# Kernel tuning notes

Hardware: AMD Instinct MI355X
Metric: run time of the kernel (lower is better)

The kernel has to match this reference:

```python
import jax, jax.numpy as jnp
import numpy as np

EMBED = 1024  # embed_dim = hidden_dim = out_dim (n_head=1)
NQ, NK = 4096, 4096
NEG = 1e16


def setup_inputs() -> dict:
    key = jax.random.key(0)
    ks = jax.random.split(key, 10)
    stdv = 1.0 / np.sqrt(EMBED)
    lin = lambda kk: jax.random.uniform(kk, (EMBED, EMBED), jnp.float32, -stdv, stdv)
    vec = lambda kk: jax.random.uniform(kk, (EMBED,), jnp.float32, -stdv, stdv)
    return {
        "q": jax.random.normal(ks[0], (NQ, EMBED), jnp.float32),
        "k": jax.random.normal(ks[1], (NK, EMBED), jnp.float32),
        "mask": jax.random.randint(ks[2], (NQ, NK), 0, 2, jnp.int32),
        "wei": jax.random.uniform(ks[3], (NQ, NK), jnp.float32),
        "Wq": lin(ks[4]), "bq": vec(ks[5]),
        "Wk": lin(ks[6]), "bk": vec(ks[7]),
        "Wp": lin(ks[8]), "bp": vec(ks[9]),
    }


def reference(q, k, mask, wei, Wq, bq, Wk, bk, Wp, bp):
    # Linear projections (torch Linear: x @ W.T + b)
    kx = k @ Wk.T + bk                      # [NK, D]
    qx = q @ Wq.T + bq                      # [NQ, D]
    # dot_product score
    score = qx @ kx.T                       # [NQ, NK]
    bias = (mask.astype(jnp.int32) - 1).astype(score.dtype) * NEG
    score = jax.nn.softmax(score + bias, axis=-1)
    # second weighted+masked softmax pass
    score = jax.nn.softmax(score * wei + bias, axis=-1)
    out = (score @ kx) @ Wp.T + bp          # [NQ, D]
    return out, score
```

## Files before the change

### kernel.cpp

```cpp
#include <hip/hip_runtime.h>


typedef __bf16 bf16;
typedef __bf16 bf16x8 __attribute__((ext_vector_type(8)));
typedef __bf16 bf16x4 __attribute__((ext_vector_type(4)));
typedef float  f32x4  __attribute__((ext_vector_type(4)));
typedef float  f32x16 __attribute__((ext_vector_type(16)));
typedef int    i32x4  __attribute__((ext_vector_type(4)));

typedef __attribute__((address_space(1))) void as1_void;
typedef __attribute__((address_space(3))) void as3_void;

#define NQ  4096
#define NKK 4096
#define EMB 1024

#define BM 128
#define BN 128
#define BK 32

__device__ __forceinline__ void gld_lds16(const void* g, void* l) {
    __builtin_amdgcn_global_load_lds((as1_void*)g, (as3_void*)l, 16, 0, 0);
}

__global__ __launch_bounds__(256) void prep_all(
    const float* __restrict__ q, const float* __restrict__ k,
    const float* __restrict__ Wq, const float* __restrict__ Wk, const float* __restrict__ Wp,
    bf16* __restrict__ qh, bf16* __restrict__ ql,
    bf16* __restrict__ kh, bf16* __restrict__ kl,
    bf16* __restrict__ Wqh, bf16* __restrict__ Wql,
    bf16* __restrict__ Wkh, bf16* __restrict__ Wkl,
    bf16* __restrict__ Wph, bf16* __restrict__ Wpl,
    int nqk, int nw)
{
    const int z = blockIdx.y;
    const float* s; bf16* h; bf16* l; int n;
    switch (z) {
        case 0:  s = q;  h = qh;  l = ql;  n = nqk; break;
        case 1:  s = k;  h = kh;  l = kl;  n = nqk; break;
        case 2:  s = Wq; h = Wqh; l = Wql; n = nw;  break;
        case 3:  s = Wk; h = Wkh; l = Wkl; n = nw;  break;
        default: s = Wp; h = Wph; l = Wpl; n = nw;  break;
    }
    const int i = (blockIdx.x * 256 + threadIdx.x) * 4;
    if (i >= n) return;
    f32x4 v = *(const f32x4*)(s + i);
    bf16x4 hv, lv;
#pragma unroll
    for (int c = 0; c < 4; c++) {
        float x = v[c];
        bf16 hh = (bf16)x;
        hv[c] = hh;
        lv[c] = (bf16)(x - (float)hh);
    }
    *(bf16x4*)(h + i) = hv;
    *(bf16x4*)(l + i) = lv;
}

template<int NS, int MODE>
__global__ __launch_bounds__(256) void reduce_k(
    const float* __restrict__ P, const float* __restrict__ bias,
    float* __restrict__ of, bf16* __restrict__ oh, int n, int Nld)
{
    const int i = (blockIdx.x * 256 + threadIdx.x) * 4;
    if (i >= n) return;
    f32x4 v = *(const f32x4*)(P + i);
#pragma unroll
    for (int s = 1; s < NS; s++)
        v += *(const f32x4*)(P + (size_t)s * n + i);
    if (MODE == 1)
        v += *(const f32x4*)(bias + (i & (Nld - 1)));
    if (MODE == 0) {
        bf16x4 o;
#pragma unroll
        for (int c = 0; c < 4; c++) o[c] = (bf16)v[c];
        *(bf16x4*)(oh + i) = o;
    } else {
        *(f32x4*)(of + i) = v;
    }
}

template<int NSPLIT, int HAS_BIAS, int OUT_BF16>
__global__ __launch_bounds__(256) void gemm_bt(
    const bf16* __restrict__ A, const bf16* __restrict__ B,
    const float* __restrict__ bias,
    float* __restrict__ Cf, bf16* __restrict__ Cb,
    int M, int N, int Ksub, int lda, int ldb)
{
    __shared__ bf16 sA[BM * BK];
    __shared__ bf16 sB[BN * BK];
    const int t    = threadIdx.x;
    const int wave = t >> 6;
    const int lane = t & 63;
    const int l31  = lane & 31;
    const int lhi  = lane >> 5;
    const int wm   = wave >> 1;
    const int wn   = wave & 1;
    const int bm   = blockIdx.y * BM;
    const int bn   = blockIdx.x * BN;
    const int srow = t >> 2;
    const int gseg = (t & 3) ^ ((srow >> 1) & 3) ^ ((srow >> 3) & 3);
    const int rsw  = ((l31 >> 1) & 3) ^ ((l31 >> 3) & 3);
    const int kz   = (NSPLIT > 0) ? (int)blockIdx.z : 0;

    A += (size_t)kz * Ksub;
    B += (size_t)kz * Ksub;
    if (NSPLIT > 0) Cf += (size_t)kz * M * N;

    const bf16* ga = A + (size_t)(bm + srow) * lda + gseg * 8;
    const bf16* gb = B + (size_t)(bn + srow) * ldb + gseg * 8;
    char* lA = (char*)sA + wave * 1024;
    char* lB = (char*)sB + wave * 1024;

    f32x16 acc[2][2] = {};

    for (int k0 = 0; k0 < Ksub; k0 += BK) {
        __syncthreads();
        gld_lds16(ga + k0,                      lA);
        gld_lds16(ga + (size_t)64 * lda + k0,   lA + 4096);
        gld_lds16(gb + k0,                      lB);
        gld_lds16(gb + (size_t)64 * ldb + k0,   lB + 4096);
        __syncthreads();
        bf16x8 af[2][2], bfr[2][2];
#pragma unroll
        for (int mi = 0; mi < 2; mi++)
#pragma unroll
            for (int kh = 0; kh < 2; kh++)
                af[mi][kh] = *(const bf16x8*)
                    &sA[(wm * 64 + mi * 32 + l31) * BK + ((kh * 2 + lhi) ^ rsw) * 8];
#pragma unroll
        for (int nj = 0; nj < 2; nj++)
#pragma unroll
            for (int kh = 0; kh < 2; kh++)
                bfr[nj][kh] = *(const bf16x8*)
                    &sB[(wn * 64 + nj * 32 + l31) * BK + ((kh * 2 + lhi) ^ rsw) * 8];
#pragma unroll
        for (int kh = 0; kh < 2; kh++)
#pragma unroll
            for (int mi = 0; mi < 2; mi++)
#pragma unroll
                for (int nj = 0; nj < 2; nj++)
                    acc[mi][nj] = __builtin_amdgcn_mfma_f32_32x32x16_bf16(
                        af[mi][kh], bfr[nj][kh], acc[mi][nj], 0, 0, 0);
    }

#pragma unroll
    for (int mi = 0; mi < 2; mi++)
#pragma unroll
        for (int nj = 0; nj < 2; nj++) {
            const int cg = bn + wn * 64 + nj * 32 + l31;
            const float bv = HAS_BIAS ? bias[cg] : 0.0f;
#pragma unroll
            for (int r = 0; r < 16; r++) {
                const int rg = bm + wm * 64 + mi * 32 + (r & 3) + 8 * (r >> 2) + 4 * lhi;
                const float v = acc[mi][nj][r] + bv;
                const size_t idx = (size_t)rg * N + cg;
                if (NSPLIT > 0)    Cf[idx] = v;
                else if (OUT_BF16) Cb[idx] = (bf16)v;
                else               Cf[idx] = v;
            }
        }
}

template<int BATCH, int HAS_BIAS, int HILO>
__global__ __launch_bounds__(256) void gemm_bt_split(
    const bf16* __restrict__ Ah0, const bf16* __restrict__ Al0,
    const bf16* __restrict__ Bh0, const bf16* __restrict__ Bl0,
    const float* __restrict__ bias0, bf16* __restrict__ Ch0, bf16* __restrict__ Cl0,
    const bf16* __restrict__ Ah1, const bf16* __restrict__ Al1,
    const bf16* __restrict__ Bh1, const bf16* __restrict__ Bl1,
    const float* __restrict__ bias1, bf16* __restrict__ Ch1, bf16* __restrict__ Cl1,
    float* __restrict__ Cf,
    int M, int N, int K)
{
    __shared__ bf16 sAh[BM * BK], sAl[BM * BK], sBh[BN * BK], sBl[BN * BK];
    const int t    = threadIdx.x;
    const int wave = t >> 6;
    const int lane = t & 63;
    const int l31  = lane & 31;
    const int lhi  = lane >> 5;
    const int wm   = wave >> 1;
    const int wn   = wave & 1;
    const int bm   = blockIdx.y * BM;
    const int bn   = blockIdx.x * BN;
    const int srow = t >> 2;
    const int gseg = (t & 3) ^ ((srow >> 1) & 3) ^ ((srow >> 3) & 3);
    const int rsw  = ((l31 >> 1) & 3) ^ ((l31 >> 3) & 3);

    const int mt = BATCH ? (int)blockIdx.z : 0;

    const bf16* Ah = (BATCH && mt) ? Ah1 : Ah0;
    const bf16* Al = (BATCH && mt) ? Al1 : Al0;
    const bf16* Bh = (BATCH && mt) ? Bh1 : Bh0;
    const bf16* Bl = (BATCH && mt) ? Bl1 : Bl0;
    const float* bias = (BATCH && mt) ? bias1 : bias0;
    bf16* Ch = (BATCH && mt) ? Ch1 : Ch0;
    bf16* Cl = (BATCH && mt) ? Cl1 : Cl0;

    const size_t offA = (size_t)(bm + srow) * K + gseg * 8;
    const size_t offB = (size_t)(bn + srow) * K + gseg * 8;
    char* lAh = (char*)sAh + wave * 1024;
    char* lAl = (char*)sAl + wave * 1024;
    char* lBh = (char*)sBh + wave * 1024;
    char* lBl = (char*)sBl + wave * 1024;

    f32x16 acc[2][2] = {};

    for (int k0 = 0; k0 < K; k0 += BK) {
        __syncthreads();
        gld_lds16(Ah + offA + k0,                  lAh);
        gld_lds16(Ah + offA + (size_t)64 * K + k0, lAh + 4096);
        gld_lds16(Al + offA + k0,                  lAl);
        gld_lds16(Al + offA + (size_t)64 * K + k0, lAl + 4096);
        gld_lds16(Bh + offB + k0,                  lBh);
        gld_lds16(Bh + offB + (size_t)64 * K + k0, lBh + 4096);
        gld_lds16(Bl + offB + k0,                  lBl);
        gld_lds16(Bl + offB + (size_t)64 * K + k0, lBl + 4096);
        __syncthreads();
#pragma unroll
        for (int kh = 0; kh < 2; kh++) {
            const int ksw = ((kh * 2 + lhi) ^ rsw) * 8;
            bf16x8 ah[2], al[2], bh2[2], bl2[2];
#pragma unroll
            for (int mi = 0; mi < 2; mi++) {
                const int ro = (wm * 64 + mi * 32 + l31) * BK + ksw;
                ah[mi] = *(const bf16x8*)&sAh[ro];
                al[mi] = *(const bf16x8*)&sAl[ro];
            }
#pragma unroll
            for (int nj = 0; nj < 2; nj++) {
                const int ro = (wn * 64 + nj * 32 + l31) * BK + ksw;
                bh2[nj] = *(const bf16x8*)&sBh[ro];
                bl2[nj] = *(const bf16x8*)&sBl[ro];
            }
#pragma unroll
            for (int mi = 0; mi < 2; mi++)
#pragma unroll
                for (int nj = 0; nj < 2; nj++) {
                    acc[mi][nj] = __builtin_amdgcn_mfma_f32_32x32x16_bf16(al[mi], bh2[nj], acc[mi][nj], 0, 0, 0);
                    acc[mi][nj] = __builtin_amdgcn_mfma_f32_32x32x16_bf16(ah[mi], bl2[nj], acc[mi][nj], 0, 0, 0);
                    acc[mi][nj] = __builtin_amdgcn_mfma_f32_32x32x16_bf16(ah[mi], bh2[nj], acc[mi][nj], 0, 0, 0);
                }
        }
    }

#pragma unroll
    for (int mi = 0; mi < 2; mi++)
#pragma unroll
        for (int nj = 0; nj < 2; nj++) {
            const int cg = bn + wn * 64 + nj * 32 + l31;
            const float bv = HAS_BIAS ? bias[cg] : 0.0f;
#pragma unroll
            for (int r = 0; r < 16; r++) {
                const int rg = bm + wm * 64 + mi * 32 + (r & 3) + 8 * (r >> 2) + 4 * lhi;
                const float v = acc[mi][nj][r] + bv;
                const size_t idx = (size_t)rg * N + cg;
                if (HILO) {
                    const bf16 hh = (bf16)v;
                    Ch[idx] = hh;
                    Cl[idx] = (bf16)(v - (float)hh);
                } else {
                    Cf[idx] = v;
                }
            }
        }
}

__global__ __launch_bounds__(512, 2) void gemm_score256(
    const bf16* __restrict__ Ah, const bf16* __restrict__ Al,
    const bf16* __restrict__ Bh, const bf16* __restrict__ Bl,
    float* __restrict__ Cf,
    const bf16* __restrict__ Wp, const bf16* __restrict__ Kx,
    bf16* __restrict__ kxpT)
{
    __shared__ bf16 smem[65536];
    const int t    = threadIdx.x;
    const int wave = t >> 6;
    const int lane = t & 63;
    const int l31  = lane & 31;
    const int lhi  = lane >> 5;
    const int wm   = wave >> 2;
    const int wn   = wave & 3;
    const int bm   = (blockIdx.x >> 4) * 256;
    const int bn   = (blockIdx.x & 15) * 256;
    const int srow = t >> 2;
    const int gseg = (t & 3) ^ ((srow >> 1) & 3) ^ ((srow >> 3) & 3);
    const int rsw  = ((l31 >> 1) & 3) ^ ((l31 >> 3) & 3);
    const int K    = EMB;
    const int NT   = K / BK;

    const bf16* gAh = Ah + (size_t)(bm + srow) * K + gseg * 8;
    const bf16* gAl = Al + (size_t)(bm + srow) * K + gseg * 8;
    const bf16* gBh = Bh + (size_t)(bn + srow) * K + gseg * 8;
    const bf16* gBl = Bl + (size_t)(bn + srow) * K + gseg * 8;

    auto stageA = [&](int buf, int k0) {
        char* L = (char*)smem + buf * 65536 + wave * 1024;
        gld_lds16(gAh + k0,                   L + 0);
        gld_lds16(gAh + (size_t)128 * K + k0, L + 8192);
        gld_lds16(gAl + k0,                   L + 16384);
        gld_lds16(gAl + (size_t)128 * K + k0, L + 16384 + 8192);
    };
    auto stageB = [&](int buf, int k0) {
        char* L = (char*)smem + buf * 65536 + wave * 1024;
        gld_lds16(gBh + k0,                   L + 32768);
        gld_lds16(gBh + (size_t)128 * K + k0, L + 32768 + 8192);
        gld_lds16(gBl + k0,                   L + 49152);
        gld_lds16(gBl + (size_t)128 * K + k0, L + 49152 + 8192);
    };

    f32x16 acc[4][2] = {};

    stageA(0, 0);
    stageB(0, 0);
    asm volatile("s_waitcnt vmcnt(0)" ::: "memory");
    __builtin_amdgcn_s_barrier();

    for (int tt = 0; tt < NT; ++tt) {
        const int cur = tt & 1;
        const int cb  = cur * 32768;
        const int kn  = (tt + 1) * BK;
        bf16x8 bh2[2], bl2[2];
#pragma unroll
        for (int ph = 0; ph < 4; ++ph) {
            const int kh   = ph >> 1;
            const int half = ph & 1;
            const int ksw  = ((kh * 2 + lhi) ^ rsw) * 8;
            if (half == 0) {
#pragma unroll
                for (int nj = 0; nj < 2; nj++) {
                    const int ro = cb + 16384 + (wn * 64 + nj * 32 + l31) * BK + ksw;
                    bh2[nj] = *(const bf16x8*)&smem[ro];
                    bl2[nj] = *(const bf16x8*)&smem[ro + 8192];
                }
            }
            bf16x8 a_h[2], a_l[2];
#pragma unroll
            for (int i = 0; i < 2; i++) {
                const int ro = cb + (wm * 128 + (half * 2 + i) * 32 + l31) * BK + ksw;
                a_h[i] = *(const bf16x8*)&smem[ro];
                a_l[i] = *(const bf16x8*)&smem[ro + 8192];
            }
            if (tt < NT - 1) {
                if (ph == 0)      stageA(cur ^ 1, kn);
                else if (ph == 1) stageB(cur ^ 1, kn);
            }
            __builtin_amdgcn_s_barrier();
            asm volatile("s_waitcnt lgkmcnt(0)" ::: "memory");
            __builtin_amdgcn_sched_barrier(0);
            __builtin_amdgcn_s_setprio(1);
#pragma unroll
            for (int i = 0; i < 2; i++) {
                const int mi = half * 2 + i;
#pragma unroll
                for (int nj = 0; nj < 2; nj++) {
                    acc[mi][nj] = __builtin_amdgcn_mfma_f32_32x32x16_bf16(a_l[i], bh2[nj], acc[mi][nj], 0, 0, 0);
                    acc[mi][nj] = __builtin_amdgcn_mfma_f32_32x32x16_bf16(a_h[i], bl2[nj], acc[mi][nj], 0, 0, 0);
                    acc[mi][nj] = __builtin_amdgcn_mfma_f32_32x32x16_bf16(a_h[i], bh2[nj], acc[mi][nj], 0, 0, 0);
                }
            }
            __builtin_amdgcn_s_setprio(0);
            if (ph == 3)
                asm volatile("s_waitcnt vmcnt(0)" ::: "memory");
            __builtin_amdgcn_s_barrier();
        }
    }

#pragma unroll
    for (int mi = 0; mi < 4; mi++)
#pragma unroll
        for (int nj = 0; nj < 2; nj++) {
            const int cg = bn + wn * 64 + nj * 32 + l31;
#pragma unroll
            for (int r = 0; r < 16; r++) {
                const int rg = bm + wm * 128 + mi * 32 + (r & 3) + 8 * (r >> 2) + 4 * lhi;
                Cf[(size_t)rg * NKK + cg] = acc[mi][nj][r];
            }
        }

    {
        const int km  = (blockIdx.x >> 5) * 128;
        const int kn2 = (blockIdx.x & 31) * 128;
        const int wm4 = wave >> 1;
        const int wn2 = wave & 1;
        const bf16* gW = Wp + (size_t)(km  + srow) * K + gseg * 8;
        const bf16* gX = Kx + (size_t)(kn2 + srow) * K + gseg * 8;
        auto stageK = [&](int buf, int k0) {
            char* L = (char*)smem + buf * 16384 + wave * 1024;
            gld_lds16(gW + k0, L);
            gld_lds16(gX + k0, L + 8192);
        };
        f32x16 ac2[2] = {};
        stageK(0, 0);
        for (int it = 0; it < NT; ++it) {
            const int cur = it & 1;
            const int cb  = cur * 8192;
            if (it < NT - 1) {
                stageK(cur ^ 1, (it + 1) * BK);
                asm volatile("s_waitcnt vmcnt(2)" ::: "memory");
            } else {
                asm volatile("s_waitcnt vmcnt(0)" ::: "memory");
            }
            __builtin_amdgcn_s_barrier();
#pragma unroll
            for (int kh = 0; kh < 2; kh++) {
                const int ksw = ((kh * 2 + lhi) ^ rsw) * 8;
                bf16x8 av  = *(const bf16x8*)&smem[cb + (wm4 * 32 + l31) * BK + ksw];
                bf16x8 bv0 = *(const bf16x8*)&smem[cb + 4096 + (wn2 * 64 + l31) * BK + ksw];
                bf16x8 bv1 = *(const bf16x8*)&smem[cb + 4096 + (wn2 * 64 + 32 + l31) * BK + ksw];
                ac2[0] = __builtin_amdgcn_mfma_f32_32x32x16_bf16(av, bv0, ac2[0], 0, 0, 0);
                ac2[1] = __builtin_amdgcn_mfma_f32_32x32x16_bf16(av, bv1, ac2[1], 0, 0, 0);
            }
            asm volatile("s_waitcnt lgkmcnt(0)" ::: "memory");
            __builtin_amdgcn_s_barrier();
        }
#pragma unroll
        for (int nj = 0; nj < 2; nj++) {
            const int cg = kn2 + wn2 * 64 + nj * 32 + l31;
#pragma unroll
            for (int r = 0; r < 16; r++) {
                const int rg = km + wm4 * 32 + (r & 3) + 8 * (r >> 2) + 4 * lhi;
                kxpT[(size_t)rg * NKK + cg] = (bf16)ac2[nj][r];
            }
        }
    }
}

__device__ __forceinline__ float wred_max(float v) {
#pragma unroll
    for (int off = 32; off > 0; off >>= 1) v = fmaxf(v, __shfl_xor(v, off));
    return v;
}
__device__ __forceinline__ float wred_sum(float v) {
#pragma unroll
    for (int off = 32; off > 0; off >>= 1) v += __shfl_xor(v, off);
    return v;
}

__global__ __launch_bounds__(256) void softmax2_kernel(
    float* __restrict__ score, const int* __restrict__ mask,
    const float* __restrict__ wei, bf16* __restrict__ scoreb)
{
    __shared__ float sred[4];
    const int row = blockIdx.x;
    const int t   = threadIdx.x;
    const size_t base = (size_t)row * NKK + (size_t)t * 16;
    const int wv = t >> 6, ln = t & 63;

    float l[16], w[16];
    unsigned mb = 0;
#pragma unroll
    for (int c = 0; c < 4; c++) {
        *(f32x4*)(l + 4 * c) = *(const f32x4*)(score + base + 4 * c);
        *(f32x4*)(w + 4 * c) = *(const f32x4*)(wei + base + 4 * c);
        i32x4 mv = *(const i32x4*)(mask + base + 4 * c);
#pragma unroll
        for (int j = 0; j < 4; j++) if (mv[j] != 0) mb |= 1u << (4 * c + j);
    }

    float mx = -__builtin_inff();
#pragma unroll
    for (int s = 0; s < 16; s++) if (mb & (1u << s)) mx = fmaxf(mx, l[s]);
    mx = wred_max(mx);
    if (ln == 0) sred[wv] = mx;
    __syncthreads();
    mx = fmaxf(fmaxf(sred[0], sred[1]), fmaxf(sred[2], sred[3]));
    __syncthreads();
    float sum = 0.f;
#pragma unroll
    for (int s = 0; s < 16; s++) {
        const float e = (mb & (1u << s)) ? __expf(l[s] - mx) : 0.f;
        l[s] = e; sum += e;
    }
    sum = wred_sum(sum);
    if (ln == 0) sred[wv] = sum;
    __syncthreads();
    sum = sred[0] + sred[1] + sred[2] + sred[3];
    __syncthreads();
    const float inv1 = 1.0f / sum;

#pragma unroll
    for (int s = 0; s < 16; s++) l[s] = l[s] * inv1 * w[s];

    float mx2 = -__builtin_inff();
#pragma unroll
    for (int s = 0; s < 16; s++) if (mb & (1u << s)) mx2 = fmaxf(mx2, l[s]);
    mx2 = wred_max(mx2);
    if (ln == 0) sred[wv] = mx2;
    __syncthreads();
    mx2 = fmaxf(fmaxf(sred[0], sred[1]), fmaxf(sred[2], sred[3]));
    __syncthreads();
    float sum2 = 0.f;
#pragma unroll
    for (int s = 0; s < 16; s++) {
        const float e = (mb & (1u << s)) ? __expf(l[s] - mx2) : 0.f;
        l[s] = e; sum2 += e;
    }
    sum2 = wred_sum(sum2);
    if (ln == 0) sred[wv] = sum2;
    __syncthreads();
    sum2 = sred[0] + sred[1] + sred[2] + sred[3];
    const float inv2 = 1.0f / sum2;

#pragma unroll
    for (int c = 0; c < 4; c++) {
        f32x4 pv;
#pragma unroll
        for (int j = 0; j < 4; j++) pv[j] = l[4 * c + j] * inv2;
        __builtin_nontemporal_store(pv, (f32x4*)(score + base + 4 * c));
#pragma unroll
        for (int j = 0; j < 4; j++) l[4 * c + j] = pv[j];
    }
    bf16x8 b0, b1;
#pragma unroll
    for (int j = 0; j < 8; j++) { b0[j] = (bf16)l[j]; b1[j] = (bf16)l[8 + j]; }
    *(bf16x8*)(scoreb + base)     = b0;
    *(bf16x8*)(scoreb + base + 8) = b1;
}

extern "C" void kernel_launch(void* const* d_in, const int* in_sizes, int n_in,
                              void* d_out, int out_size, void* d_ws, size_t ws_size,
                              hipStream_t stream)
{
    (void)in_sizes; (void)n_in; (void)out_size;
    const float* q    = (const float*)d_in[0];
    const float* k    = (const float*)d_in[1];
    const int*   mask = (const int*)  d_in[2];
    const float* wei  = (const float*)d_in[3];
    const float* Wq   = (const float*)d_in[4];
    const float* bq   = (const float*)d_in[5];
    const float* Wk   = (const float*)d_in[6];
    const float* bk   = (const float*)d_in[7];
    const float* Wp   = (const float*)d_in[8];
    const float* bp   = (const float*)d_in[9];

    float* out   = (float*)d_out;
    float* score = (float*)d_out + (size_t)NQ * EMB;

    char* ws = (char*)d_ws;
    size_t off = 0;
    auto alloc = [&](size_t bytes) -> char* {
        char* p = ws + off; off += (bytes + 255) & ~(size_t)255; return p;
    };
    const size_t n_qk = (size_t)NQ * EMB;
    const size_t n_w  = (size_t)EMB * EMB;
    const size_t n_sc = (size_t)NQ * NKK;

    bf16* qh   = (bf16*)alloc(n_qk * 2);
    bf16* ql   = (bf16*)alloc(n_qk * 2);
    bf16* kh   = (bf16*)alloc(n_qk * 2);
    bf16* kl   = (bf16*)alloc(n_qk * 2);
    bf16* qxh  = (bf16*)alloc(n_qk * 2);
    bf16* qxl  = (bf16*)alloc(n_qk * 2);
    bf16* kxh  = (bf16*)alloc(n_qk * 2);
    bf16* kxl  = (bf16*)alloc(n_qk * 2);
    bf16* Wqh  = (bf16*)alloc(n_w * 2);
    bf16* Wql  = (bf16*)alloc(n_w * 2);
    bf16* Wkh  = (bf16*)alloc(n_w * 2);
    bf16* Wkl  = (bf16*)alloc(n_w * 2);
    bf16* Wpb  = (bf16*)alloc(n_w * 2);
    bf16* Wpl  = (bf16*)alloc(n_w * 2);
    bf16* kxpTb = (bf16*)alloc(n_qk * 2);
    bf16* scoreb = (bf16*)alloc(n_sc * 2);
    const size_t base_off = off;
    float* P = (float*)alloc(2 * n_qk * 4);
    const bool ws_ok = (off <= ws_size);
    if (base_off > ws_size) return;

    const int MN = (int)n_qk;

    prep_all<<<dim3(n_qk / 1024, 5), 256, 0, stream>>>(
        q, k, Wq, Wk, Wp,
        qh, ql, kh, kl, Wqh, Wql, Wkh, Wkl, Wpb, Wpl,
        (int)n_qk, (int)n_w);

    gemm_bt_split<1, 1, 1><<<dim3(EMB / BN, NQ / BM, 2), 256, 0, stream>>>(
        qh, ql, Wqh, Wql, bq, qxh, qxl,
        kh, kl, Wkh, Wkl, bk, kxh, kxl,
        nullptr, NQ, EMB, EMB);

    gemm_score256<<<dim3(256), 512, 0, stream>>>(
        qxh, qxl, kxh, kxl, score, Wpb, kxh, kxpTb);

    softmax2_kernel<<<dim3(NQ), 256, 0, stream>>>(score, mask, wei, scoreb);

    if (ws_ok) {
        gemm_bt<2, 0, 0><<<dim3(EMB / BN, NQ / BM, 2), 256, 0, stream>>>(
            scoreb, kxpTb, nullptr, P, nullptr, NQ, EMB, NKK / 2, NKK, NKK);
        reduce_k<2, 1><<<dim3(MN / 1024), 256, 0, stream>>>(
            P, bp, out, nullptr, MN, EMB);
    } else {
        gemm_bt<0, 1, 0><<<dim3(EMB / BN, NQ / BM), 256, 0, stream>>>(
            scoreb, kxpTb, bp, out, nullptr, NQ, EMB, NKK, NKK, NKK);
    }
}
```

Measured before the change: 476.9 us.

## Rework score GEMM into 4-stage BK=16 LDS pipeline with one barrier per tile

The score GEMM main loop goes from a double-buffered BK=32 scheme with four barrier phases per tile to a four-buffer ring of BK=16 tiles. Three tiles are prefetched ahead and vmcnt waits are used instead of full drains. Each tile now needs one barrier and one batch of LDS reads feeding 24 MFMAs. The LDS layout drops the XOR swizzle for a plain 16-element row layout, which may cause LDS bank conflicts on the fragment reads.

Result: no change. 485.0 us (+1.7%).

```diff
diff --git a/kernel.cpp b/kernel.cpp
--- a/kernel.cpp
+++ b/kernel.cpp
@@ -283,88 +283,77 @@
     const int wn   = wave & 3;
     const int bm   = (blockIdx.x >> 4) * 256;
     const int bn   = (blockIdx.x & 15) * 256;
-    const int srow = t >> 2;
-    const int gseg = (t & 3) ^ ((srow >> 1) & 3) ^ ((srow >> 3) & 3);
-    const int rsw  = ((l31 >> 1) & 3) ^ ((l31 >> 3) & 3);
     const int K    = EMB;
-    const int NT   = K / BK;
-
-    const bf16* gAh = Ah + (size_t)(bm + srow) * K + gseg * 8;
-    const bf16* gAl = Al + (size_t)(bm + srow) * K + gseg * 8;
-    const bf16* gBh = Bh + (size_t)(bn + srow) * K + gseg * 8;
-    const bf16* gBl = Bl + (size_t)(bn + srow) * K + gseg * 8;
-
-    auto stageA = [&](int buf, int k0) {
-        char* L = (char*)smem + buf * 65536 + wave * 1024;
-        gld_lds16(gAh + k0,                   L + 0);
-        gld_lds16(gAh + (size_t)128 * K + k0, L + 8192);
-        gld_lds16(gAl + k0,                   L + 16384);
-        gld_lds16(gAl + (size_t)128 * K + k0, L + 16384 + 8192);
+
+    const int strow = wave * 32 + (lane >> 1);
+    const int stcol = (lane & 1) * 8;
+    const bf16* gAh = Ah + (size_t)(bm + strow) * K + stcol;
+    const bf16* gAl = Al + (size_t)(bm + strow) * K + stcol;
+    const bf16* gBh = Bh + (size_t)(bn + strow) * K + stcol;
+    const bf16* gBl = Bl + (size_t)(bn + strow) * K + stcol;
+
+    auto stage = [&](int sbB, int tt) {
+        char* L = (char*)smem + sbB + wave * 1024;
+        const int ko = tt * 16;
+        gld_lds16(gAh + ko, L);
+        gld_lds16(gAl + ko, L + 8192);
+        gld_lds16(gBh + ko, L + 16384);
+        gld_lds16(gBl + ko, L + 24576);
     };
-    auto stageB = [&](int buf, int k0) {
-        char* L = (char*)smem + buf * 65536 + wave * 1024;
-        gld_lds16(gBh + k0,                   L + 32768);
-        gld_lds16(gBh + (size_t)128 * K + k0, L + 32768 + 8192);
-        gld_lds16(gBl + k0,                   L + 49152);
-        gld_lds16(gBl + (size_t)128 * K + k0, L + 49152 + 8192);
+
+    f32x16 acc[4][2] = {};
+
+    const int aoff = (wm * 128 + l31) * 16 + lhi * 8;
+    const int boff = 8192 + (wn * 64 + l31) * 16 + lhi * 8;
+
+    auto tile_body = [&](int cbE, int sbB, int stt, bool do_stage) {
+        __builtin_amdgcn_s_barrier();
+        if (do_stage) stage(sbB, stt);
+        bf16x8 a_h[4], a_l[4], b_h[2], b_l[2];
+#pragma unroll
+        for (int mi = 0; mi < 4; mi++) {
+            a_h[mi] = *(const bf16x8*)&smem[cbE + aoff + mi * 512];
+            a_l[mi] = *(const bf16x8*)&smem[cbE + 4096 + aoff + mi * 512];
+        }
+#pragma unroll
+        for (int nj = 0; nj < 2; nj++) {
+            b_h[nj] = *(const bf16x8*)&smem[cbE + boff + nj * 512];
+            b_l[nj] = *(const bf16x8*)&smem[cbE + 4096 + boff + nj * 512];
+        }
+        asm volatile("s_waitcnt lgkmcnt(0)" ::: "memory");
+        __builtin_amdgcn_sched_barrier(0);
+        __builtin_amdgcn_s_setprio(1);
+#pragma unroll
+        for (int mi = 0; mi < 4; mi++)
+#pragma unroll
+            for (int nj = 0; nj < 2; nj++) {
+                acc[mi][nj] = __builtin_amdgcn_mfma_f32_32x32x16_bf16(a_l[mi], b_h[nj], acc[mi][nj], 0, 0, 0);
+                acc[mi][nj] = __builtin_amdgcn_mfma_f32_32x32x16_bf16(a_h[mi], b_l[nj], acc[mi][nj], 0, 0, 0);
+                acc[mi][nj] = __builtin_amdgcn_mfma_f32_32x32x16_bf16(a_h[mi], b_h[nj], acc[mi][nj], 0, 0, 0);
+            }
+        __builtin_amdgcn_s_setprio(0);
     };
 
-    f32x16 acc[4][2] = {};
-
-    stageA(0, 0);
-    stageB(0, 0);
-    asm volatile("s_waitcnt vmcnt(0)" ::: "memory");
-    __builtin_amdgcn_s_barrier();
-
-    for (int tt = 0; tt < NT; ++tt) {
-        const int cur = tt & 1;
-        const int cb  = cur * 32768;
-        const int kn  = (tt + 1) * BK;
-        bf16x8 bh2[2], bl2[2];
-#pragma unroll
-        for (int ph = 0; ph < 4; ++ph) {
-            const int kh   = ph >> 1;
-            const int half = ph & 1;
-            const int ksw  = ((kh * 2 + lhi) ^ rsw) * 8;
-            if (half == 0) {
-#pragma unroll
-                for (int nj = 0; nj < 2; nj++) {
-                    const int ro = cb + 16384 + (wn * 64 + nj * 32 + l31) * BK + ksw;
-                    bh2[nj] = *(const bf16x8*)&smem[ro];
-                    bl2[nj] = *(const bf16x8*)&smem[ro + 8192];
-                }
-            }
-            bf16x8 a_h[2], a_l[2];
-#pragma unroll
-            for (int i = 0; i < 2; i++) {
-                const int ro = cb + (wm * 128 + (half * 2 + i) * 32 + l31) * BK + ksw;
-                a_h[i] = *(const bf16x8*)&smem[ro];
-                a_l[i] = *(const bf16x8*)&smem[ro + 8192];
-            }
-            if (tt < NT - 1) {
-                if (ph == 0)      stageA(cur ^ 1, kn);
-                else if (ph == 1) stageB(cur ^ 1, kn);
-            }
-            __builtin_amdgcn_s_barrier();
-            asm volatile("s_waitcnt lgkmcnt(0)" ::: "memory");
-            __builtin_amdgcn_sched_barrier(0);
-            __builtin_amdgcn_s_setprio(1);
-#pragma unroll
-            for (int i = 0; i < 2; i++) {
-                const int mi = half * 2 + i;
-#pragma unroll
-                for (int nj = 0; nj < 2; nj++) {
-                    acc[mi][nj] = __builtin_amdgcn_mfma_f32_32x32x16_bf16(a_l[i], bh2[nj], acc[mi][nj], 0, 0, 0);
-                    acc[mi][nj] = __builtin_amdgcn_mfma_f32_32x32x16_bf16(a_h[i], bl2[nj], acc[mi][nj], 0, 0, 0);
-                    acc[mi][nj] = __builtin_amdgcn_mfma_f32_32x32x16_bf16(a_h[i], bh2[nj], acc[mi][nj], 0, 0, 0);
-                }
-            }
-            __builtin_amdgcn_s_setprio(0);
-            if (ph == 3)
-                asm volatile("s_waitcnt vmcnt(0)" ::: "memory");
-            __builtin_amdgcn_s_barrier();
-        }
-    }
+#define VW8 asm volatile("s_waitcnt vmcnt(8)" ::: "memory")
+#define VW4 asm volatile("s_waitcnt vmcnt(4)" ::: "memory")
+#define VW0 asm volatile("s_waitcnt vmcnt(0)" ::: "memory")
+
+    stage(0, 0); stage(32768, 1); stage(65536, 2);
+
+    for (int tb = 0; tb < 60; tb += 4) {
+        VW8; tile_body(    0,  98304, tb + 3, true);
+        VW8; tile_body(16384,      0, tb + 4, true);
+        VW8; tile_body(32768,  32768, tb + 5, true);
+        VW8; tile_body(49152,  65536, tb + 6, true);
+    }
+    VW8; tile_body(    0,  98304, 63, true);
+    VW8; tile_body(16384,      0,  0, false);
+    VW4; tile_body(32768,      0,  0, false);
+    VW0; tile_body(49152,      0,  0, false);
+
+#undef VW8
+#undef VW4
+#undef VW0
 
 #pragma unroll
     for (int mi = 0; mi < 4; mi++)
@@ -379,10 +368,14 @@
         }
 
     {
+        const int srow = t >> 2;
+        const int gseg = (t & 3) ^ ((srow >> 1) & 3) ^ ((srow >> 3) & 3);
+        const int rsw  = ((l31 >> 1) & 3) ^ ((l31 >> 3) & 3);
         const int km  = (blockIdx.x >> 5) * 128;
         const int kn2 = (blockIdx.x & 31) * 128;
         const int wm4 = wave >> 1;
         const int wn2 = wave & 1;
+        const int NT2 = K / BK;
         const bf16* gW = Wp + (size_t)(km  + srow) * K + gseg * 8;
         const bf16* gX = Kx + (size_t)(kn2 + srow) * K + gseg * 8;
         auto stageK = [&](int buf, int k0) {
@@ -392,10 +385,10 @@
         };
         f32x16 ac2[2] = {};
         stageK(0, 0);
-        for (int it = 0; it < NT; ++it) {
+        for (int it = 0; it < NT2; ++it) {
             const int cur = it & 1;
             const int cb  = cur * 8192;
-            if (it < NT - 1) {
+            if (it < NT2 - 1) {
                 stageK(cur ^ 1, (it + 1) * BK);
                 asm volatile("s_waitcnt vmcnt(2)" ::: "memory");
             } else {
```
